# Performance work log

Hardware: AMD Instinct MI355X
Metric: run time of the kernel (lower is better)

## Reference

```python
import jax, jax.numpy as jnp
import numpy as np
import math

HEADS = 16
D_MODEL = 1024
D_K = D_MODEL // HEADS


def setup_inputs() -> dict:
    key = jax.random.key(0)
    ks = jax.random.split(key, 11)
    B, S = 2, 2048
    s = 1.0 / math.sqrt(D_MODEL)
    return {
        "q": jax.random.normal(ks[0], (B, S, D_MODEL), jnp.float32),
        "k": jax.random.normal(ks[1], (B, S, D_MODEL), jnp.float32),
        "v": jax.random.normal(ks[2], (B, S, D_MODEL), jnp.float32),
        "Wq": jax.random.normal(ks[3], (D_MODEL, D_MODEL), jnp.float32) * s,
        "bq": jax.random.normal(ks[4], (D_MODEL,), jnp.float32) * s,
        "Wk": jax.random.normal(ks[5], (D_MODEL, D_MODEL), jnp.float32) * s,
        "bk": jax.random.normal(ks[6], (D_MODEL,), jnp.float32) * s,
        "Wv": jax.random.normal(ks[7], (D_MODEL, D_MODEL), jnp.float32) * s,
        "bv": jax.random.normal(ks[8], (D_MODEL,), jnp.float32) * s,
        "Wo": jax.random.normal(ks[9], (D_MODEL, D_MODEL), jnp.float32) * s,
        "bo": jax.random.normal(ks[10], (D_MODEL,), jnp.float32) * s,
    }


def reference(q, k, v, Wq, bq, Wk, bk, Wv, bv, Wo, bo):
    B, S, _ = q.shape
    # linear projections, split heads: [B, H, S, d_k]
    def proj(x, W, b):
        y = x @ W.T + b
        return y.reshape(B, -1, HEADS, D_K).transpose(0, 2, 1, 3)
    qh, kh, vh = proj(q, Wq, bq), proj(k, Wk, bk), proj(v, Wv, bv)
    # abs-modified scaled dot-product attention (no mask, eval -> no dropout)
    scores = jnp.abs(jnp.einsum("bhsd,bhtd->bhst", qh, kh) / math.sqrt(D_K))
    attn = jax.nn.softmax(scores, axis=-1)
    out = jnp.einsum("bhst,bhtd->bhsd", attn, vh)
    concat = out.transpose(0, 2, 1, 3).reshape(B, S, D_MODEL)
    return concat @ Wo.T + bo
```

## Files before the change

### kernel.cpp

```cpp
#include <hip/hip_runtime.h>
#include <hip/hip_bf16.h>

#define HEADS 16
#define DK 64
#define DM 1024
#define SEQ 2048
#define BATCH 2

using bf16x8 = __attribute__((ext_vector_type(8))) short;
using short4v = __attribute__((ext_vector_type(4))) short;
using f32x4 = __attribute__((ext_vector_type(4))) float;

static __device__ __forceinline__ short f2bf(float x) {
  union { float f; unsigned u; } c;
  c.f = x;
  unsigned r = (c.u + 0x7FFFu + ((c.u >> 16) & 1u)) >> 16;
  return (short)r;
}

static __device__ __forceinline__ unsigned pk2bf(float lo, float hi) {
  union { __hip_bfloat162 h; unsigned u; } c;
  c.h = __float22bfloat162_rn(float2{lo, hi});
  return c.u;
}

static __device__ __forceinline__ void gload_lds16(const void* g, void* l) {
  __builtin_amdgcn_global_load_lds(
      (const __attribute__((address_space(1))) void*)g,
      (__attribute__((address_space(3))) void*)l, 16, 0, 0);
}

__global__ __launch_bounds__(256) void cvt7(
    const float* __restrict__ s0, const float* __restrict__ s1,
    const float* __restrict__ s2, const float* __restrict__ s3,
    const float* __restrict__ s4, const float* __restrict__ s5,
    const float* __restrict__ s6, short* d0, short* d1, short* d2, short* d3,
    short* d4, short* d5, short* d6) {
  const int y = blockIdx.y;
  const float* s;
  short* d;
  int n;
  switch (y) {
    case 0: s = s0; d = d0; n = BATCH * SEQ * DM; break;
    case 1: s = s1; d = d1; n = BATCH * SEQ * DM; break;
    case 2: s = s2; d = d2; n = BATCH * SEQ * DM; break;
    case 3: s = s3; d = d3; n = DM * DM; break;
    case 4: s = s4; d = d4; n = DM * DM; break;
    case 5: s = s5; d = d5; n = DM * DM; break;
    default: s = s6; d = d6; n = DM * DM; break;
  }
  const int n4 = n >> 2;
  const int stride = gridDim.x * 256;
  for (int i = blockIdx.x * 256 + threadIdx.x; i < n4; i += stride) {
    float4 v = ((const float4*)s)[i];
    short4v o;
    o.x = f2bf(v.x);
    o.y = f2bf(v.y);
    o.z = f2bf(v.z);
    o.w = f2bf(v.w);
    ((short4v*)d)[i] = o;
  }
}

__global__ __launch_bounds__(256) void proj_qkv(
    const short* __restrict__ Aq, const short* __restrict__ Ak,
    const short* __restrict__ Av, const short* __restrict__ Wq_,
    const short* __restrict__ Wk_, const short* __restrict__ Wv_,
    const float* __restrict__ bq, const float* __restrict__ bk,
    const float* __restrict__ bv, short* __restrict__ Qh,
    short* __restrict__ Kh, short* __restrict__ Vt) {
  __shared__ short smem[12288];
  short* As = smem;
  short* Ws = smem + 4096;

  const int z = blockIdx.z;
  const short* A = z == 0 ? Aq : z == 1 ? Ak : Av;
  const short* W = z == 0 ? Wq_ : z == 1 ? Wk_ : Wv_;
  const float* bias = z == 0 ? bq : z == 1 ? bk : bv;
  short* C = z == 0 ? Qh : z == 1 ? Kh : Vt;
  const bool tr = (z == 2);

  const int tid = threadIdx.x;
  const int wave = tid >> 6, lane = tid & 63;
  const int quad = lane >> 4, l15 = lane & 15;
  const int n0 = blockIdx.x * 128, m0 = blockIdx.y * 64;
  const int mh = (wave & 1) * 32, nh = (wave >> 1) * 64;
  const int ldr = lane >> 3, ldc = lane & 7;

  f32x4 acc[2][4] = {};

  for (int k0 = 0; k0 < 1024; k0 += 64) {
    __syncthreads();
#pragma unroll
    for (int i = 0; i < 6; ++i) {
      int seg = wave * 6 + i;
      if (seg < 8) {
        int r = seg * 8 + ldr;
        int kb = ldc ^ (r & 7);
        gload_lds16(&A[(size_t)(m0 + r) * 1024 + k0 + kb * 8], &As[seg * 512]);
      } else {
        int r = (seg - 8) * 8 + ldr;
        int kb = ldc ^ (r & 7);
        gload_lds16(&W[(size_t)(n0 + r) * 1024 + k0 + kb * 8],
                    &Ws[(seg - 8) * 512]);
      }
    }
    __syncthreads();
#pragma unroll
    for (int ks = 0; ks < 2; ++ks) {
      bf16x8 a[2], b[4];
      int kb = ks * 4 + quad;
#pragma unroll
      for (int f = 0; f < 2; ++f) {
        int rm = mh + f * 16 + l15;
        a[f] = *(const bf16x8*)&As[rm * 64 + (kb ^ (rm & 7)) * 8];
      }
#pragma unroll
      for (int f = 0; f < 4; ++f) {
        int rn = nh + f * 16 + l15;
        b[f] = *(const bf16x8*)&Ws[rn * 64 + (kb ^ (rn & 7)) * 8];
      }
#pragma unroll
      for (int mf = 0; mf < 2; ++mf)
#pragma unroll
        for (int nf = 0; nf < 4; ++nf)
          acc[mf][nf] = __builtin_amdgcn_mfma_f32_16x16x32_bf16(
              a[mf], b[nf], acc[mf][nf], 0, 0, 0);
    }
  }

  float bvv[4];
#pragma unroll
  for (int nf = 0; nf < 4; ++nf) bvv[nf] = bias[n0 + nh + nf * 16 + l15];

  __syncthreads();
  short* Cb = smem;

  if (!tr) {
    const float osc = (z == 0) ? 0.18033688011112042f : 1.0f;
#pragma unroll
    for (int mf = 0; mf < 2; ++mf)
#pragma unroll
      for (int nf = 0; nf < 4; ++nf)
#pragma unroll
        for (int r = 0; r < 4; ++r)
          Cb[(mh + mf * 16 + quad * 4 + r) * 136 + nh + nf * 16 + l15] =
              f2bf((acc[mf][nf][r] + bvv[nf]) * osc);
    __syncthreads();
#pragma unroll
    for (int j = 0; j < 4; ++j) {
      int cid = tid + 256 * j;
      int row = cid >> 4, cb = cid & 15;
      bf16x8 v = *(const bf16x8*)&Cb[row * 136 + cb * 8];
      int m = m0 + row, n = n0 + cb * 8;
      int b = m >> 11, s = m & (SEQ - 1), h = n >> 6, d = n & 63;
      *(bf16x8*)&C[((size_t)(b * HEADS + h) * SEQ + s) * DK + d] = v;
    }
  } else {
#pragma unroll
    for (int mf = 0; mf < 2; ++mf)
#pragma unroll
      for (int nf = 0; nf < 4; ++nf) {
        short4v p;
        p.x = f2bf(acc[mf][nf][0] + bvv[nf]);
        p.y = f2bf(acc[mf][nf][1] + bvv[nf]);
        p.z = f2bf(acc[mf][nf][2] + bvv[nf]);
        p.w = f2bf(acc[mf][nf][3] + bvv[nf]);
        *(short4v*)&Cb[(nh + nf * 16 + l15) * 72 + mh + mf * 16 + quad * 4] =
            p;
      }
    __syncthreads();
#pragma unroll
    for (int j = 0; j < 4; ++j) {
      int cid = tid + 256 * j;
      int row = cid >> 3, cb = cid & 7;
      bf16x8 v = *(const bf16x8*)&Cb[row * 72 + cb * 8];
      int n = n0 + row, m = m0 + cb * 8;
      int b = m >> 11, s = m & (SEQ - 1), h = n >> 6, d = n & 63;
      *(bf16x8*)&C[((size_t)(b * HEADS + h) * DK + d) * SEQ + s] = v;
    }
  }
}

__global__ __launch_bounds__(256) void proj_out(const short* __restrict__ A,
                                                const short* __restrict__ W,
                                                const float* __restrict__ bias,
                                                float* __restrict__ C) {
  __shared__ short smem[12288];
  short* As = smem;
  short* Ws = smem + 4096;

  const int tid = threadIdx.x;
  const int wave = tid >> 6, lane = tid & 63;
  const int quad = lane >> 4, l15 = lane & 15;
  const int n0 = blockIdx.x * 128, m0 = blockIdx.y * 64;
  const int mh = (wave & 1) * 32, nh = (wave >> 1) * 64;
  const int ldr = lane >> 3, ldc = lane & 7;

  f32x4 acc[2][4] = {};

  for (int k0 = 0; k0 < 1024; k0 += 64) {
    __syncthreads();
#pragma unroll
    for (int i = 0; i < 6; ++i) {
      int seg = wave * 6 + i;
      if (seg < 8) {
        int r = seg * 8 + ldr;
        int kb = ldc ^ (r & 7);
        gload_lds16(&A[(size_t)(m0 + r) * 1024 + k0 + kb * 8], &As[seg * 512]);
      } else {
        int r = (seg - 8) * 8 + ldr;
        int kb = ldc ^ (r & 7);
        gload_lds16(&W[(size_t)(n0 + r) * 1024 + k0 + kb * 8],
                    &Ws[(seg - 8) * 512]);
      }
    }
    __syncthreads();
#pragma unroll
    for (int ks = 0; ks < 2; ++ks) {
      bf16x8 a[2], b[4];
      int kb = ks * 4 + quad;
#pragma unroll
      for (int f = 0; f < 2; ++f) {
        int rm = mh + f * 16 + l15;
        a[f] = *(const bf16x8*)&As[rm * 64 + (kb ^ (rm & 7)) * 8];
      }
#pragma unroll
      for (int f = 0; f < 4; ++f) {
        int rn = nh + f * 16 + l15;
        b[f] = *(const bf16x8*)&Ws[rn * 64 + (kb ^ (rn & 7)) * 8];
      }
#pragma unroll
      for (int mf = 0; mf < 2; ++mf)
#pragma unroll
        for (int nf = 0; nf < 4; ++nf)
          acc[mf][nf] = __builtin_amdgcn_mfma_f32_16x16x32_bf16(
              a[mf], b[nf], acc[mf][nf], 0, 0, 0);
    }
  }

  float bvv[4];
#pragma unroll
  for (int nf = 0; nf < 4; ++nf) bvv[nf] = bias[n0 + nh + nf * 16 + l15];
#pragma unroll
  for (int mf = 0; mf < 2; ++mf)
#pragma unroll
    for (int nf = 0; nf < 4; ++nf)
#pragma unroll
      for (int r = 0; r < 4; ++r)
        C[(size_t)(m0 + mh + mf * 16 + quad * 4 + r) * 1024 + n0 + nh +
          nf * 16 + l15] = acc[mf][nf][r] + bvv[nf];
}

__global__ __launch_bounds__(512, 4) void attn_mfma(
    const short* __restrict__ Qh, const short* __restrict__ Kh,
    const short* __restrict__ VtG, short* __restrict__ concat) {
  __shared__ __align__(16) short smem[4 * 64 * 64];
  __shared__ float Lsm[128];
  short* Kbuf = smem;
  short* Vbuf = smem + 2 * 4096;

  const int tid = threadIdx.x;
  const int wave = tid >> 6, lane = tid & 63;
  const int quad = lane >> 4, l15 = lane & 15;
  const int wq = wave & 3;
  const int wg = wave >> 2;
  const int lin = blockIdx.x + (blockIdx.y << 4);
  const int o = ((lin & 7) << 6) + (lin >> 3);
  const int bh = o >> 4;
  const int q0 = (o & 15) * 128;
  const size_t base = (size_t)bh * SEQ * DK;
  const int ldr = lane >> 3, ldc = lane & 7;
  const int NT = SEQ / 64;

  bf16x8 qf[2][2];
#pragma unroll
  for (int mf = 0; mf < 2; ++mf)
#pragma unroll
    for (int ks = 0; ks < 2; ++ks)
      qf[mf][ks] =
          *(const bf16x8*)&Qh[base +
                              (size_t)(q0 + wq * 32 + mf * 16 + l15) * 64 +
                              ks * 32 + quad * 8];

  bf16x8 ones;
#pragma unroll
  for (int i = 0; i < 8; ++i) ones[i] = (short)0x3F80;

  f32x4 O[2][4] = {};
  f32x4 Lacc[2] = {};

  int krow[2];
#pragma unroll
  for (int kfl = 0; kfl < 2; ++kfl)
    krow[kfl] = 32 * wg + 8 * (l15 >> 2) + 4 * kfl + (l15 & 3);

  auto stage = [&](int kt, int buf) {
    int r = wave * 8 + ldr;
    int kswz = (r & 7) ^ (((r >> 3) & 3) << 1);
    gload_lds16(&Kh[base + (size_t)(kt * 64 + r) * 64 + (ldc ^ kswz) * 8],
                &Kbuf[buf * 4096 + wave * 512]);
    gload_lds16(&VtG[base + (size_t)r * SEQ + kt * 64 + (ldc ^ (r & 7)) * 8],
                &Vbuf[buf * 4096 + wave * 512]);
  };

  stage(0, 0);
  __syncthreads();

  int cur = 0;
  for (int kt = 0; kt < NT; ++kt) {
    if (kt + 1 < NT) stage(kt + 1, cur ^ 1);

    const short* Ks = &Kbuf[cur * 4096];
    const short* Vs = &Vbuf[cur * 4096];

    f32x4 sf[2][2] = {};
#pragma unroll
    for (int ks = 0; ks < 2; ++ks) {
      bf16x8 kfr[2];
      int kb = ks * 4 + quad;
#pragma unroll
      for (int kfl = 0; kfl < 2; ++kfl) {
        int n = krow[kfl];
        int kswz = (n & 7) ^ (((n >> 3) & 3) << 1);
        kfr[kfl] = *(const bf16x8*)&Ks[n * 64 + ((kb ^ kswz) << 3)];
      }
      __builtin_amdgcn_s_setprio(1);
#pragma unroll
      for (int kfl = 0; kfl < 2; ++kfl)
#pragma unroll
        for (int mf = 0; mf < 2; ++mf)
          sf[mf][kfl] = __builtin_amdgcn_mfma_f32_16x16x32_bf16(
              kfr[kfl], qf[mf][ks], sf[mf][kfl], 0, 0, 0);
      __builtin_amdgcn_s_setprio(0);
    }

    bf16x8 pa[2];
#pragma unroll
    for (int mf = 0; mf < 2; ++mf) {
      float e[8];
#pragma unroll
      for (int kfl = 0; kfl < 2; ++kfl)
#pragma unroll
        for (int r = 0; r < 4; ++r)
          e[kfl * 4 + r] = __builtin_amdgcn_exp2f(fabsf(sf[mf][kfl][r]));
      union { unsigned u[4]; bf16x8 v; } t;
      t.u[0] = pk2bf(e[0], e[1]);
      t.u[1] = pk2bf(e[2], e[3]);
      t.u[2] = pk2bf(e[4], e[5]);
      t.u[3] = pk2bf(e[6], e[7]);
      pa[mf] = t.v;
    }

    {
      int gb = wg * 4 + quad;
      bf16x8 bvf[4];
#pragma unroll
      for (int nf = 0; nf < 4; ++nf) {
        int d = nf * 16 + l15;
        bvf[nf] = *(const bf16x8*)&Vs[d * 64 + ((gb ^ (d & 7)) << 3)];
      }
      __builtin_amdgcn_s_setprio(1);
#pragma unroll
      for (int mf = 0; mf < 2; ++mf) {
#pragma unroll
        for (int nf = 0; nf < 4; ++nf)
          O[mf][nf] = __builtin_amdgcn_mfma_f32_16x16x32_bf16(
              pa[mf], bvf[nf], O[mf][nf], 0, 0, 0);
        Lacc[mf] = __builtin_amdgcn_mfma_f32_16x16x32_bf16(pa[mf], ones,
                                                           Lacc[mf], 0, 0, 0);
      }
      __builtin_amdgcn_s_setprio(0);
    }

    __syncthreads();
    cur ^= 1;
  }

  float* Osm = (float*)smem;
  if (wg == 1) {
#pragma unroll
    for (int mf = 0; mf < 2; ++mf)
#pragma unroll
      for (int nf = 0; nf < 4; ++nf) {
        int d = nf * 16 + l15;
        int rowb = (wq * 32 + mf * 16 + quad * 4) ^ ((d & 7) << 2);
        *(f32x4*)&Osm[d * 128 + rowb] = O[mf][nf];
      }
    if (l15 == 0)
#pragma unroll
      for (int mf = 0; mf < 2; ++mf)
#pragma unroll
        for (int r = 0; r < 4; ++r)
          Lsm[wq * 32 + mf * 16 + quad * 4 + r] = Lacc[mf][r];
  }
  __syncthreads();

  float inv_[2][4];
  if (wg == 0) {
#pragma unroll
    for (int mf = 0; mf < 2; ++mf)
#pragma unroll
      for (int nf = 0; nf < 4; ++nf) {
        int d = nf * 16 + l15;
        int rowb = (wq * 32 + mf * 16 + quad * 4) ^ ((d & 7) << 2);
        O[mf][nf] += *(const f32x4*)&Osm[d * 128 + rowb];
      }
#pragma unroll
    for (int mf = 0; mf < 2; ++mf)
#pragma unroll
      for (int r = 0; r < 4; ++r)
        inv_[mf][r] =
            1.f / (Lacc[mf][r] + Lsm[wq * 32 + mf * 16 + quad * 4 + r]);
  }
  __syncthreads();

  short* Es = smem;
  if (wg == 0) {
#pragma unroll
    for (int mf = 0; mf < 2; ++mf)
#pragma unroll
      for (int nf = 0; nf < 4; ++nf)
#pragma unroll
        for (int r = 0; r < 4; ++r) {
          int rw = wq * 32 + mf * 16 + quad * 4 + r;
          int d = nf * 16 + l15;
          Es[rw * 64 + (((d >> 3) ^ (rw & 7)) << 3) + (d & 7)] =
              f2bf(O[mf][nf][r] * inv_[mf][r]);
        }
  }
  __syncthreads();
  const int b = bh >> 4, h = bh & 15;
#pragma unroll
  for (int j = 0; j < 2; ++j) {
    int cid = tid + 512 * j;
    int rw = cid >> 3, g = cid & 7;
    bf16x8 v = *(const bf16x8*)&Es[rw * 64 + ((g ^ (rw & 7)) << 3)];
    *(bf16x8*)&concat[((size_t)(b * SEQ + q0 + rw)) * DM + h * 64 + g * 8] = v;
  }
}

extern "C" void kernel_launch(void* const* d_in, const int* in_sizes, int n_in,
                              void* d_out, int out_size, void* d_ws,
                              size_t ws_size, hipStream_t stream) {
  const float* q = (const float*)d_in[0];
  const float* k = (const float*)d_in[1];
  const float* v = (const float*)d_in[2];
  const float* Wq = (const float*)d_in[3];
  const float* bq = (const float*)d_in[4];
  const float* Wk = (const float*)d_in[5];
  const float* bk = (const float*)d_in[6];
  const float* Wv = (const float*)d_in[7];
  const float* bv = (const float*)d_in[8];
  const float* Wo = (const float*)d_in[9];
  const float* bo = (const float*)d_in[10];

  short* ws = (short*)d_ws;
  const size_t T4 = (size_t)BATCH * SEQ * DM;
  const size_t T1 = (size_t)DM * DM;
  short* qb = ws;
  short* kb_ = ws + T4;
  short* vb = ws + 2 * T4;
  short* Wqb = ws + 3 * T4;
  short* Wkb = Wqb + T1;
  short* Wvb = Wqb + 2 * T1;
  short* Wob = Wqb + 3 * T1;
  short* Qh = Wqb + 4 * T1;
  short* Kh = Qh + T4;
  short* VtG = Qh + 2 * T4;
  short* cc = Qh + 3 * T4;

  cvt7<<<dim3(1024, 7), 256, 0, stream>>>(q, k, v, Wq, Wk, Wv, Wo, qb, kb_, vb,
                                          Wqb, Wkb, Wvb, Wob);

  proj_qkv<<<dim3(DM / 128, (BATCH * SEQ) / 64, 3), 256, 0, stream>>>(
      qb, kb_, vb, Wqb, Wkb, Wvb, bq, bk, bv, Qh, Kh, VtG);

  attn_mfma<<<dim3(SEQ / 128, BATCH * HEADS), 512, 0, stream>>>(Qh, Kh, VtG,
                                                                cc);

  proj_out<<<dim3(DM / 128, (BATCH * SEQ) / 64), 256, 0, stream>>>(
      cc, Wob, bo, (float*)d_out);
}
```

Measured before the change: 225.6 us.

## Split K across two wave groups in output projection with LDS reduction

The output projection block grows from 256 to 512 threads. Each half of the waves handles half of the K dimension using its own LDS buffers, and the partial sums are reduced through shared memory before the bias-add and store. The aim is more waves per tile and a shorter serial K loop, giving better latency hiding in a kernel that has few blocks. The cost is twice the LDS, an extra reduction pass with two barriers, and half the threads sitting idle during the epilogue.

After: 221.0 us. 2.0% less time.

```diff
diff --git a/kernel.cpp b/kernel.cpp
--- a/kernel.cpp
+++ b/kernel.cpp
@@ -182,28 +182,30 @@
   }
 }
 
-__global__ __launch_bounds__(256) void proj_out(const short* __restrict__ A,
+__global__ __launch_bounds__(512) void proj_out(const short* __restrict__ A,
                                                 const short* __restrict__ W,
                                                 const float* __restrict__ bias,
                                                 float* __restrict__ C) {
-  __shared__ short smem[12288];
-  short* As = smem;
-  short* Ws = smem + 4096;
+  __shared__ short smem[2][12288];
 
   const int tid = threadIdx.x;
-  const int wave = tid >> 6, lane = tid & 63;
+  const int w8 = tid >> 6, lane = tid & 63;
+  const int wk2 = w8 >> 2, wv = w8 & 3;
   const int quad = lane >> 4, l15 = lane & 15;
   const int n0 = blockIdx.x * 128, m0 = blockIdx.y * 64;
-  const int mh = (wave & 1) * 32, nh = (wave >> 1) * 64;
+  const int mh = (wv & 1) * 32, nh = (wv >> 1) * 64;
   const int ldr = lane >> 3, ldc = lane & 7;
+  short* As = smem[wk2];
+  short* Ws = smem[wk2] + 4096;
 
   f32x4 acc[2][4] = {};
 
-  for (int k0 = 0; k0 < 1024; k0 += 64) {
+  for (int kk = 0; kk < 8; ++kk) {
+    const int k0 = wk2 * 512 + kk * 64;
     __syncthreads();
 #pragma unroll
     for (int i = 0; i < 6; ++i) {
-      int seg = wave * 6 + i;
+      int seg = wv * 6 + i;
       if (seg < 8) {
         int r = seg * 8 + ldr;
         int kb = ldc ^ (r & 7);
@@ -239,17 +241,37 @@
     }
   }
 
-  float bvv[4];
-#pragma unroll
-  for (int nf = 0; nf < 4; ++nf) bvv[nf] = bias[n0 + nh + nf * 16 + l15];
-#pragma unroll
-  for (int mf = 0; mf < 2; ++mf)
-#pragma unroll
-    for (int nf = 0; nf < 4; ++nf)
-#pragma unroll
-      for (int r = 0; r < 4; ++r)
-        C[(size_t)(m0 + mh + mf * 16 + quad * 4 + r) * 1024 + n0 + nh +
-          nf * 16 + l15] = acc[mf][nf][r] + bvv[nf];
+  __syncthreads();
+  float* Osm = (float*)&smem[0][0];
+  if (wk2 == 1) {
+#pragma unroll
+    for (int mf = 0; mf < 2; ++mf)
+#pragma unroll
+      for (int nf = 0; nf < 4; ++nf)
+#pragma unroll
+        for (int r = 0; r < 4; ++r) {
+          int row = mh + mf * 16 + quad * 4 + r;
+          int col = nh + nf * 16 + l15;
+          Osm[row * 132 + col] = acc[mf][nf][r];
+        }
+  }
+  __syncthreads();
+  if (wk2 == 0) {
+    float bvv[4];
+#pragma unroll
+    for (int nf = 0; nf < 4; ++nf) bvv[nf] = bias[n0 + nh + nf * 16 + l15];
+#pragma unroll
+    for (int mf = 0; mf < 2; ++mf)
+#pragma unroll
+      for (int nf = 0; nf < 4; ++nf)
+#pragma unroll
+        for (int r = 0; r < 4; ++r) {
+          int row = mh + mf * 16 + quad * 4 + r;
+          int col = nh + nf * 16 + l15;
+          C[(size_t)(m0 + row) * 1024 + n0 + col] =
+              acc[mf][nf][r] + Osm[row * 132 + col] + bvv[nf];
+        }
+  }
 }
 
 __global__ __launch_bounds__(512, 4) void attn_mfma(
@@ -479,6 +501,6 @@
   attn_mfma<<<dim3(SEQ / 128, BATCH * HEADS), 512, 0, stream>>>(Qh, Kh, VtG,
                                                                 cc);
 
-  proj_out<<<dim3(DM / 128, (BATCH * SEQ) / 64), 256, 0, stream>>>(
+  proj_out<<<dim3(DM / 128, (BATCH * SEQ) / 64), 512, 0, stream>>>(
       cc, Wob, bo, (float*)d_out);
 }
```

## Fuse activation fp32-to-bf16 conversion into QKV projection loads

Applied to the files above, without the earlier changes.

The separate conversion pass over q, k and v is removed. The projection kernel now reads the fp32 activations straight from global memory into registers, packs them to bf16 and stores them swizzled into LDS. Only the weights still go through a shortened conversion kernel, which now does one float4 per thread with no grid-stride loop. This cuts a full read and write of three 16 MB tensors, but each projection block now re-reads fp32 A tiles (twice the bytes per tile), and register staging replaces the async LDS loads for A.

Measured after the change: 229.0 us. About the same (+1.5%).

```diff
diff --git a/kernel.cpp b/kernel.cpp
--- a/kernel.cpp
+++ b/kernel.cpp
@@ -30,41 +30,26 @@
       (__attribute__((address_space(3))) void*)l, 16, 0, 0);
 }
 
-__global__ __launch_bounds__(256) void cvt7(
+__global__ __launch_bounds__(256) void cvt4(
     const float* __restrict__ s0, const float* __restrict__ s1,
-    const float* __restrict__ s2, const float* __restrict__ s3,
-    const float* __restrict__ s4, const float* __restrict__ s5,
-    const float* __restrict__ s6, short* d0, short* d1, short* d2, short* d3,
-    short* d4, short* d5, short* d6) {
+    const float* __restrict__ s2, const float* __restrict__ s3, short* d0,
+    short* d1, short* d2, short* d3) {
   const int y = blockIdx.y;
-  const float* s;
-  short* d;
-  int n;
-  switch (y) {
-    case 0: s = s0; d = d0; n = BATCH * SEQ * DM; break;
-    case 1: s = s1; d = d1; n = BATCH * SEQ * DM; break;
-    case 2: s = s2; d = d2; n = BATCH * SEQ * DM; break;
-    case 3: s = s3; d = d3; n = DM * DM; break;
-    case 4: s = s4; d = d4; n = DM * DM; break;
-    case 5: s = s5; d = d5; n = DM * DM; break;
-    default: s = s6; d = d6; n = DM * DM; break;
-  }
-  const int n4 = n >> 2;
-  const int stride = gridDim.x * 256;
-  for (int i = blockIdx.x * 256 + threadIdx.x; i < n4; i += stride) {
-    float4 v = ((const float4*)s)[i];
-    short4v o;
-    o.x = f2bf(v.x);
-    o.y = f2bf(v.y);
-    o.z = f2bf(v.z);
-    o.w = f2bf(v.w);
-    ((short4v*)d)[i] = o;
-  }
+  const float* s = y == 0 ? s0 : y == 1 ? s1 : y == 2 ? s2 : s3;
+  short* d = y == 0 ? d0 : y == 1 ? d1 : y == 2 ? d2 : d3;
+  const int i = blockIdx.x * 256 + threadIdx.x;
+  float4 v = ((const float4*)s)[i];
+  short4v o;
+  o.x = f2bf(v.x);
+  o.y = f2bf(v.y);
+  o.z = f2bf(v.z);
+  o.w = f2bf(v.w);
+  ((short4v*)d)[i] = o;
 }
 
 __global__ __launch_bounds__(256) void proj_qkv(
-    const short* __restrict__ Aq, const short* __restrict__ Ak,
-    const short* __restrict__ Av, const short* __restrict__ Wq_,
+    const float* __restrict__ Aq, const float* __restrict__ Ak,
+    const float* __restrict__ Av, const short* __restrict__ Wq_,
     const short* __restrict__ Wk_, const short* __restrict__ Wv_,
     const float* __restrict__ bq, const float* __restrict__ bk,
     const float* __restrict__ bv, short* __restrict__ Qh,
@@ -74,7 +59,7 @@
   short* Ws = smem + 4096;
 
   const int z = blockIdx.z;
-  const short* A = z == 0 ? Aq : z == 1 ? Ak : Av;
+  const float* A = z == 0 ? Aq : z == 1 ? Ak : Av;
   const short* W = z == 0 ? Wq_ : z == 1 ? Wk_ : Wv_;
   const float* bias = z == 0 ? bq : z == 1 ? bk : bv;
   short* C = z == 0 ? Qh : z == 1 ? Kh : Vt;
@@ -90,20 +75,33 @@
   f32x4 acc[2][4] = {};
 
   for (int k0 = 0; k0 < 1024; k0 += 64) {
-    __syncthreads();
-#pragma unroll
-    for (int i = 0; i < 6; ++i) {
-      int seg = wave * 6 + i;
-      if (seg < 8) {
-        int r = seg * 8 + ldr;
-        int kb = ldc ^ (r & 7);
-        gload_lds16(&A[(size_t)(m0 + r) * 1024 + k0 + kb * 8], &As[seg * 512]);
-      } else {
-        int r = (seg - 8) * 8 + ldr;
-        int kb = ldc ^ (r & 7);
-        gload_lds16(&W[(size_t)(n0 + r) * 1024 + k0 + kb * 8],
-                    &Ws[(seg - 8) * 512]);
-      }
+    float4 av0[2], av1[2];
+#pragma unroll
+    for (int i = 0; i < 2; ++i) {
+      int seg = wave * 2 + i;
+      int r = seg * 8 + ldr;
+      int kb = ldc ^ (r & 7);
+      const float* src = &A[(size_t)(m0 + r) * 1024 + k0 + kb * 8];
+      av0[i] = *(const float4*)src;
+      av1[i] = *(const float4*)(src + 4);
+    }
+    __syncthreads();
+#pragma unroll
+    for (int i = 0; i < 2; ++i) {
+      int seg = wave * 2 + i;
+      union { unsigned u[4]; bf16x8 v; } t;
+      t.u[0] = pk2bf(av0[i].x, av0[i].y);
+      t.u[1] = pk2bf(av0[i].z, av0[i].w);
+      t.u[2] = pk2bf(av1[i].x, av1[i].y);
+      t.u[3] = pk2bf(av1[i].z, av1[i].w);
+      *(bf16x8*)&As[seg * 512 + lane * 8] = t.v;
+    }
+#pragma unroll
+    for (int i = 0; i < 4; ++i) {
+      int seg = wave * 4 + i;
+      int r = seg * 8 + ldr;
+      int kb = ldc ^ (r & 7);
+      gload_lds16(&W[(size_t)(n0 + r) * 1024 + k0 + kb * 8], &Ws[seg * 512]);
     }
     __syncthreads();
 #pragma unroll
@@ -458,9 +456,6 @@
   short* ws = (short*)d_ws;
   const size_t T4 = (size_t)BATCH * SEQ * DM;
   const size_t T1 = (size_t)DM * DM;
-  short* qb = ws;
-  short* kb_ = ws + T4;
-  short* vb = ws + 2 * T4;
   short* Wqb = ws + 3 * T4;
   short* Wkb = Wqb + T1;
   short* Wvb = Wqb + 2 * T1;
@@ -470,11 +465,10 @@
   short* VtG = Qh + 2 * T4;
   short* cc = Qh + 3 * T4;
 
-  cvt7<<<dim3(1024, 7), 256, 0, stream>>>(q, k, v, Wq, Wk, Wv, Wo, qb, kb_, vb,
-                                          Wqb, Wkb, Wvb, Wob);
+  cvt4<<<dim3(1024, 4), 256, 0, stream>>>(Wq, Wk, Wv, Wo, Wqb, Wkb, Wvb, Wob);
 
   proj_qkv<<<dim3(DM / 128, (BATCH * SEQ) / 64, 3), 256, 0, stream>>>(
-      qb, kb_, vb, Wqb, Wkb, Wvb, bq, bk, bv, Qh, Kh, VtG);
+      q, k, v, Wqb, Wkb, Wvb, bq, bk, bv, Qh, Kh, VtG);
 
   attn_mfma<<<dim3(SEQ / 128, BATCH * HEADS), 512, 0, stream>>>(Qh, Kh, VtG,
                                                                 cc);
```
